# Kernel optimization log

Hardware: AMD Instinct MI355X
Metric: run time of the kernel (lower is better)

Reference implementation:

```python
import jax, jax.numpy as jnp
import numpy as np

ALPHA = 1.0 / 10.0  # dt / tau

def setup_inputs() -> dict:
    key = jax.random.key(0)
    ks = jax.random.split(key, 5)
    seq_len, batch, input_dim, hidden = 256, 128, 256, 1024
    return {
        "input": jax.random.normal(ks[0], (seq_len, batch, input_dim), dtype=jnp.float32),
        "W_in": jax.random.normal(ks[1], (hidden, input_dim), dtype=jnp.float32) / np.sqrt(input_dim),
        "b_in": jax.random.normal(ks[2], (hidden,), dtype=jnp.float32) * 0.01,
        "W_hh": jax.random.normal(ks[3], (hidden, hidden), dtype=jnp.float32) / np.sqrt(hidden),
        "b_hh": jax.random.normal(ks[4], (hidden,), dtype=jnp.float32) * 0.01,
        "h0": jnp.zeros((hidden,), dtype=jnp.float32),
    }

def reference(input, W_in, b_in, W_hh, b_hh, h0):
    # input: [T, B, I] -> states: [T, B, H]
    # Precompute input projections for all timesteps (linear, same math as per-step).
    x_proj = jnp.einsum('tbi,hi->tbh', input, W_in) + b_in  # [T, B, H]
    h_init = jnp.broadcast_to(h0, (input.shape[1], h0.shape[0]))  # [B, H]

    def step(h, xp):
        rec = h @ W_hh.T + b_hh                       # [B, H]
        h_new = (1.0 - ALPHA) * h + ALPHA * (rec + xp)  # leaky integration (noise sigma = 0)
        h_new = jax.nn.relu(h_new)
        return h_new, h_new

    _, states = jax.lax.scan(step, h_init, x_proj)
    return states  # [T, B, H]
```

## Files before the change

### kernel.cpp

```cpp
#include <hip/hip_runtime.h>
#include <hip/hip_bf16.h>

#define T_LEN 256
#define B_DIM 128
#define I_DIM 256
#define H_DIM 1024

typedef __attribute__((ext_vector_type(8))) short short8;
typedef __attribute__((ext_vector_type(4))) float f32x4;

__device__ unsigned g_sync[256];

static __device__ __forceinline__ unsigned short f2bf(float f) {
  unsigned u = __float_as_uint(f);
  return (unsigned short)((u + 0x7fffu + ((u >> 16) & 1u)) >> 16);
}

__global__ __launch_bounds__(256) void xproj_gemm(
    const float* __restrict__ A, const float* __restrict__ W,
    const float* __restrict__ bias, float* __restrict__ C) {
  __shared__ float As[64][33];
  __shared__ float Ws[64][33];

  const int tid = threadIdx.x;
  const int m0 = blockIdx.y * 64;
  const int n0 = blockIdx.x * 64;
  const int ty = tid >> 4;
  const int tx = tid & 15;
  const int r   = tid >> 3;
  const int c4  = (tid & 7) << 2;

  float acc[4][4] = {};

  for (int kc = 0; kc < I_DIM; kc += 32) {
#pragma unroll
    for (int p = 0; p < 2; ++p) {
      const int rr = r + p * 32;
      const float4 a = *(const float4*)(A + (size_t)(m0 + rr) * I_DIM + kc + c4);
      As[rr][c4 + 0] = a.x; As[rr][c4 + 1] = a.y;
      As[rr][c4 + 2] = a.z; As[rr][c4 + 3] = a.w;
      const float4 w = *(const float4*)(W + (size_t)(n0 + rr) * I_DIM + kc + c4);
      Ws[rr][c4 + 0] = w.x; Ws[rr][c4 + 1] = w.y;
      Ws[rr][c4 + 2] = w.z; Ws[rr][c4 + 3] = w.w;
    }
    __syncthreads();
#pragma unroll
    for (int k = 0; k < 32; ++k) {
      float av[4], wv[4];
#pragma unroll
      for (int i = 0; i < 4; ++i) av[i] = As[ty * 4 + i][k];
#pragma unroll
      for (int j = 0; j < 4; ++j) wv[j] = Ws[tx * 4 + j][k];
#pragma unroll
      for (int i = 0; i < 4; ++i)
#pragma unroll
        for (int j = 0; j < 4; ++j)
          acc[i][j] = fmaf(av[i], wv[j], acc[i][j]);
    }
    __syncthreads();
  }

  const float4 bv = *(const float4*)(bias + n0 + tx * 4);
#pragma unroll
  for (int i = 0; i < 4; ++i) {
    float4 o;
    o.x = acc[i][0] + bv.x;
    o.y = acc[i][1] + bv.y;
    o.z = acc[i][2] + bv.z;
    o.w = acc[i][3] + bv.w;
    *(float4*)(C + (size_t)(m0 + ty * 4 + i) * H_DIM + n0 + tx * 4) = o;
  }
}

__global__ __launch_bounds__(256) void cvt_w_bf16(
    const float* __restrict__ W, unsigned short* __restrict__ Wb) {
  const int i4 = blockIdx.x * 256 + threadIdx.x;
  const float4 w = ((const float4*)W)[i4];
  ushort4 o;
  o.x = f2bf(w.x); o.y = f2bf(w.y); o.z = f2bf(w.z); o.w = f2bf(w.w);
  ((ushort4*)Wb)[i4] = o;
}

__global__ __launch_bounds__(256) void init_hT0(
    const float* __restrict__ h0, unsigned short* __restrict__ hT) {
  const int idx = blockIdx.x * 256 + threadIdx.x;
  hT[idx] = f2bf(h0[idx & (H_DIM - 1)]);
  if (blockIdx.x == 0) g_sync[threadIdx.x] = 0u;
}

__global__ __launch_bounds__(256, 1) void rnn_persist(
    unsigned short* __restrict__ hT,
    const unsigned short* __restrict__ Wb,
    const float* __restrict__ b_hh,
    const float* __restrict__ h0,
    float* __restrict__ out)
{
  __shared__ float red[2][16][33];

  const int tid  = threadIdx.x;
  const int wv   = tid >> 6;
  const int lane = tid & 63;
  const int ln   = lane & 15;
  const int q    = lane >> 4;

  const int bid = blockIdx.x;
  const int bq  = bid >> 5;
  const int lj  = bid & 31;
  const int j0  = lj * 32;
  const int mt  = wv & 1;
  const int kh  = wv >> 1;
  const int b0  = bq * 32 + mt * 16;

  short8 wfrag[2][16];
#pragma unroll
  for (int jf = 0; jf < 2; ++jf) {
    const short8* __restrict__ wb8 =
        (const short8*)(Wb + (size_t)(j0 + jf * 16 + ln) * H_DIM + kh * 512 + q * 8);
#pragma unroll
    for (int kc = 0; kc < 16; ++kc) wfrag[jf][kc] = wb8[kc * 4];
  }

  const size_t HT = (size_t)B_DIM * H_DIM;
  const size_t arow = (size_t)(b0 + ln) * H_DIM + kh * 512 + q * 8;
  const unsigned short* __restrict__ ha0 = hT + arow;
  const unsigned short* __restrict__ ha1 = hT + HT + arow;

  float bj[2];
#pragma unroll
  for (int jf = 0; jf < 2; ++jf) bj[jf] = b_hh[j0 + jf * 16 + ln];

  const size_t obase = (size_t)(b0 + q * 4) * H_DIM + j0 + ln;

  float hcur[2][4];
#pragma unroll
  for (int jf = 0; jf < 2; ++jf) {
    const float h0j = h0[j0 + jf * 16 + ln];
#pragma unroll
    for (int r = 0; r < 4; ++r) hcur[jf][r] = h0j;
  }

  unsigned* flags = &g_sync[bq * 32];
  unsigned* epoch = &g_sync[128 + bq * 32];

  for (int t = 0; t < T_LEN; ++t) {
#pragma unroll
    for (int jf = 0; jf < 2; ++jf)
#pragma unroll
      for (int kc = 0; kc < 16; ++kc) asm volatile("" : "+v"(wfrag[jf][kc]));

    float* __restrict__ xio_t = out + (size_t)t * HT;

    float xpv[2][4];
    if (wv < 2) {
#pragma unroll
      for (int jf = 0; jf < 2; ++jf)
#pragma unroll
        for (int r = 0; r < 4; ++r)
          xpv[jf][r] = xio_t[obase + (size_t)r * H_DIM + jf * 16];
    }

    const unsigned short* __restrict__ ha = (t & 1) ? ha1 : ha0;
    short8 hfrag[16];
#pragma unroll
    for (int kc = 0; kc < 16; ++kc) {
      asm volatile("global_load_dwordx4 %0, %1, off offset:%2 sc0 sc1"
                   : "=&v"(hfrag[kc]) : "v"(ha), "i"(kc * 64));
    }
    asm volatile("s_waitcnt vmcnt(0)" ::: "memory");
    __builtin_amdgcn_sched_barrier(0);

    f32x4 a0[2], a1[2];
#pragma unroll
    for (int jf = 0; jf < 2; ++jf) { a0[jf] = (f32x4){0,0,0,0}; a1[jf] = (f32x4){0,0,0,0}; }
#pragma unroll
    for (int kc = 0; kc < 16; kc += 2) {
#pragma unroll
      for (int jf = 0; jf < 2; ++jf) {
        a0[jf] = __builtin_amdgcn_mfma_f32_16x16x32_bf16(hfrag[kc],     wfrag[jf][kc],     a0[jf], 0, 0, 0);
        a1[jf] = __builtin_amdgcn_mfma_f32_16x16x32_bf16(hfrag[kc + 1], wfrag[jf][kc + 1], a1[jf], 0, 0, 0);
      }
    }
    f32x4 acc[2];
#pragma unroll
    for (int jf = 0; jf < 2; ++jf) acc[jf] = a0[jf] + a1[jf];

    if (wv >= 2) {
#pragma unroll
      for (int jf = 0; jf < 2; ++jf)
#pragma unroll
        for (int r = 0; r < 4; ++r) red[mt][q * 4 + r][jf * 16 + ln] = acc[jf][r];
    }
    __syncthreads();
    if (wv < 2) {
      unsigned short* __restrict__ hnext = hT + (size_t)((t + 1) & 1) * HT;
#pragma unroll
      for (int jf = 0; jf < 2; ++jf)
#pragma unroll
        for (int r = 0; r < 4; ++r) {
          const float rec = acc[jf][r] + red[mt][q * 4 + r][jf * 16 + ln];
          float v = 0.9f * hcur[jf][r] + 0.1f * (rec + bj[jf] + xpv[jf][r]);
          v = v > 0.f ? v : 0.f;
          hcur[jf][r] = v;
          const size_t oidx = obase + (size_t)r * H_DIM + jf * 16;
          xio_t[oidx] = v;
          __hip_atomic_store(&hnext[oidx], f2bf(v), __ATOMIC_RELAXED,
                             __HIP_MEMORY_SCOPE_AGENT);
        }
    }
    __syncthreads();

    const unsigned tgt = (unsigned)(t + 1);
    if (lj == 0) {
      if (wv == 0) {
        if (lane == 0)
          __hip_atomic_store(&flags[0], tgt, __ATOMIC_RELAXED,
                             __HIP_MEMORY_SCOPE_AGENT);
        unsigned* fp = &flags[lane & 31];
        for (;;) {
          unsigned fv;
          asm volatile("global_load_dword %0, %1, off sc0 sc1\n\t"
                       "s_waitcnt vmcnt(0)"
                       : "=v"(fv) : "v"(fp) : "memory");
          if (__all((int)fv >= (int)tgt)) break;
          __builtin_amdgcn_s_sleep(1);
        }
        if (lane == 0)
          __hip_atomic_store(epoch, tgt, __ATOMIC_RELAXED,
                             __HIP_MEMORY_SCOPE_AGENT);
      }
    } else if (tid == 0) {
      __hip_atomic_store(&flags[lj], tgt, __ATOMIC_RELAXED,
                         __HIP_MEMORY_SCOPE_AGENT);
      for (;;) {
        unsigned ev;
        asm volatile("global_load_dword %0, %1, off sc0 sc1\n\t"
                     "s_waitcnt vmcnt(0)"
                     : "=v"(ev) : "v"(epoch) : "memory");
        if (ev >= tgt) break;
        __builtin_amdgcn_s_sleep(1);
      }
    }
    __syncthreads();
  }
}

extern "C" void kernel_launch(void* const* d_in, const int* in_sizes, int n_in,
                              void* d_out, int out_size, void* d_ws, size_t ws_size,
                              hipStream_t stream) {
  const float* input = (const float*)d_in[0];
  const float* W_in  = (const float*)d_in[1];
  const float* b_in  = (const float*)d_in[2];
  const float* W_hh  = (const float*)d_in[3];
  const float* b_hh  = (const float*)d_in[4];
  const float* h0    = (const float*)d_in[5];
  float* out = (float*)d_out;

  unsigned short* Wb = (unsigned short*)d_ws;
  unsigned short* hT = Wb + (1 << 20);

  cvt_w_bf16<<<(H_DIM * H_DIM / 4) / 256, 256, 0, stream>>>(W_hh, Wb);
  init_hT0<<<(B_DIM * H_DIM) / 256, 256, 0, stream>>>(h0, hT);

  dim3 g1(H_DIM / 64, (T_LEN * B_DIM) / 64);
  xproj_gemm<<<g1, 256, 0, stream>>>(input, W_in, b_in, out);

  {
    unsigned short* hT_ = hT;
    const unsigned short* Wb_ = Wb;
    const float* bhh_ = b_hh;
    const float* h0_ = h0;
    float* out_ = out;
    void* pargs[5] = {(void*)&hT_, (void*)&Wb_, (void*)&bhh_, (void*)&h0_, (void*)&out_};
    hipLaunchCooperativeKernel((const void*)rnn_persist, dim3(128), dim3(256),
                               pargs, 0, stream);
  }
}
```

Baseline: 1.643 ms.

## Use split-bf16 MFMA for input projection and decentralize step barrier

The input projection GEMM moves from scalar fp32 FMA to MFMA on bf16 hi/lo split operands, using three products to keep near-fp32 accuracy. This path is taken only when the workspace is large enough, and it adds two conversion kernels. The recurrent kernel also drops its two-level barrier (leader gathers flags and publishes an epoch). Instead, each block publishes its own flag and, at the start of the next step, polls all 32 peer flags in its batch group. That removes one barrier stage and the trailing __syncthreads from each timestep.

```diff
diff --git a/kernel.cpp b/kernel.cpp
--- a/kernel.cpp
+++ b/kernel.cpp
@@ -14,6 +14,9 @@
 static __device__ __forceinline__ unsigned short f2bf(float f) {
   unsigned u = __float_as_uint(f);
   return (unsigned short)((u + 0x7fffu + ((u >> 16) & 1u)) >> 16);
+}
+static __device__ __forceinline__ float bf2f(unsigned short h) {
+  return __uint_as_float((unsigned)h << 16);
 }
 
 __global__ __launch_bounds__(256) void xproj_gemm(
@@ -72,6 +75,74 @@
   }
 }
 
+__global__ __launch_bounds__(256) void cvt_hi_lo(
+    const float* __restrict__ X, unsigned short* __restrict__ Xh,
+    unsigned short* __restrict__ Xl) {
+  const int i4 = blockIdx.x * 256 + threadIdx.x;
+  const float4 x = ((const float4*)X)[i4];
+  ushort4 h, l;
+  h.x = f2bf(x.x); l.x = f2bf(x.x - bf2f(h.x));
+  h.y = f2bf(x.y); l.y = f2bf(x.y - bf2f(h.y));
+  h.z = f2bf(x.z); l.z = f2bf(x.z - bf2f(h.z));
+  h.w = f2bf(x.w); l.w = f2bf(x.w - bf2f(h.w));
+  ((ushort4*)Xh)[i4] = h;
+  ((ushort4*)Xl)[i4] = l;
+}
+
+__global__ __launch_bounds__(256) void xproj_mfma(
+    const unsigned short* __restrict__ Ah, const unsigned short* __restrict__ Al,
+    const unsigned short* __restrict__ Wh, const unsigned short* __restrict__ Wl,
+    const float* __restrict__ bias, float* __restrict__ C) {
+  const int tid  = threadIdx.x;
+  const int wv   = tid >> 6;
+  const int lane = tid & 63;
+  const int ln   = lane & 15;
+  const int q    = lane >> 4;
+  const int mw   = wv >> 1;
+  const int nw   = wv & 1;
+  const int m0   = blockIdx.y * 128 + mw * 64;
+  const int n0   = blockIdx.x * 64  + nw * 32;
+
+  f32x4 acc[4][2] = {};
+
+#pragma unroll
+  for (int kc = 0; kc < 8; ++kc) {
+    const int ko = kc * 32 + q * 8;
+    short8 afh[4], afl[4], wfh[2], wfl[2];
+#pragma unroll
+    for (int fm = 0; fm < 4; ++fm) {
+      const size_t off = (size_t)(m0 + fm * 16 + ln) * I_DIM + ko;
+      afh[fm] = *(const short8*)(Ah + off);
+      afl[fm] = *(const short8*)(Al + off);
+    }
+#pragma unroll
+    for (int fn = 0; fn < 2; ++fn) {
+      const size_t off = (size_t)(n0 + fn * 16 + ln) * I_DIM + ko;
+      wfh[fn] = *(const short8*)(Wh + off);
+      wfl[fn] = *(const short8*)(Wl + off);
+    }
+#pragma unroll
+    for (int fm = 0; fm < 4; ++fm)
+#pragma unroll
+      for (int fn = 0; fn < 2; ++fn) {
+        acc[fm][fn] = __builtin_amdgcn_mfma_f32_16x16x32_bf16(afh[fm], wfh[fn], acc[fm][fn], 0, 0, 0);
+        acc[fm][fn] = __builtin_amdgcn_mfma_f32_16x16x32_bf16(afh[fm], wfl[fn], acc[fm][fn], 0, 0, 0);
+        acc[fm][fn] = __builtin_amdgcn_mfma_f32_16x16x32_bf16(afl[fm], wfh[fn], acc[fm][fn], 0, 0, 0);
+      }
+  }
+
+#pragma unroll
+  for (int fn = 0; fn < 2; ++fn) {
+    const int j = n0 + fn * 16 + ln;
+    const float bj = bias[j];
+#pragma unroll
+    for (int fm = 0; fm < 4; ++fm)
+#pragma unroll
+      for (int r = 0; r < 4; ++r)
+        C[(size_t)(m0 + fm * 16 + q * 4 + r) * H_DIM + j] = acc[fm][fn][r] + bj;
+  }
+}
+
 __global__ __launch_bounds__(256) void cvt_w_bf16(
     const float* __restrict__ W, unsigned short* __restrict__ Wb) {
   const int i4 = blockIdx.x * 256 + threadIdx.x;
@@ -140,7 +211,8 @@
   }
 
   unsigned* flags = &g_sync[bq * 32];
-  unsigned* epoch = &g_sync[128 + bq * 32];
+  unsigned* myflag = &g_sync[bq * 32 + lj];
+  unsigned* pollp  = &g_sync[bq * 32 + kh * 16 + ln];
 
   for (int t = 0; t < T_LEN; ++t) {
 #pragma unroll
@@ -158,6 +230,19 @@
         for (int r = 0; r < 4; ++r)
           xpv[jf][r] = xio_t[obase + (size_t)r * H_DIM + jf * 16];
     }
+
+    if (t > 0) {
+      const unsigned tgt = (unsigned)t;
+      for (;;) {
+        unsigned fv;
+        asm volatile("global_load_dword %0, %1, off sc0 sc1\n\t"
+                     "s_waitcnt vmcnt(0)"
+                     : "=v"(fv) : "v"(pollp) : "memory");
+        if (__all((int)fv >= (int)tgt)) break;
+        __builtin_amdgcn_s_sleep(1);
+      }
+    }
+    __builtin_amdgcn_sched_barrier(0);
 
     const unsigned short* __restrict__ ha = (t & 1) ? ha1 : ha0;
     short8 hfrag[16];
@@ -208,40 +293,11 @@
         }
     }
     __syncthreads();
-
-    const unsigned tgt = (unsigned)(t + 1);
-    if (lj == 0) {
-      if (wv == 0) {
-        if (lane == 0)
-          __hip_atomic_store(&flags[0], tgt, __ATOMIC_RELAXED,
-                             __HIP_MEMORY_SCOPE_AGENT);
-        unsigned* fp = &flags[lane & 31];
-        for (;;) {
-          unsigned fv;
-          asm volatile("global_load_dword %0, %1, off sc0 sc1\n\t"
-                       "s_waitcnt vmcnt(0)"
-                       : "=v"(fv) : "v"(fp) : "memory");
-          if (__all((int)fv >= (int)tgt)) break;
-          __builtin_amdgcn_s_sleep(1);
-        }
-        if (lane == 0)
-          __hip_atomic_store(epoch, tgt, __ATOMIC_RELAXED,
-                             __HIP_MEMORY_SCOPE_AGENT);
-      }
-    } else if (tid == 0) {
-      __hip_atomic_store(&flags[lj], tgt, __ATOMIC_RELAXED,
+    if (tid == 0)
+      __hip_atomic_store(myflag, (unsigned)(t + 1), __ATOMIC_RELAXED,
                          __HIP_MEMORY_SCOPE_AGENT);
-      for (;;) {
-        unsigned ev;
-        asm volatile("global_load_dword %0, %1, off sc0 sc1\n\t"
-                     "s_waitcnt vmcnt(0)"
-                     : "=v"(ev) : "v"(epoch) : "memory");
-        if (ev >= tgt) break;
-        __builtin_amdgcn_s_sleep(1);
-      }
-    }
-    __syncthreads();
-  }
+  }
+  (void)flags;
 }
 
 extern "C" void kernel_launch(void* const* d_in, const int* in_sizes, int n_in,
@@ -255,14 +311,26 @@
   const float* h0    = (const float*)d_in[5];
   float* out = (float*)d_out;
 
-  unsigned short* Wb = (unsigned short*)d_ws;
-  unsigned short* hT = Wb + (1 << 20);
+  char* ws = (char*)d_ws;
+  unsigned short* Wb  = (unsigned short*)ws;
+  unsigned short* hT  = (unsigned short*)(ws + (2u << 20));
+  unsigned short* Wih = (unsigned short*)(ws + (5u << 19));
+  unsigned short* Wil = (unsigned short*)(ws + (3u << 20));
+  unsigned short* Ah  = (unsigned short*)(ws + (4u << 20));
+  unsigned short* Al  = (unsigned short*)(ws + (20u << 20));
 
   cvt_w_bf16<<<(H_DIM * H_DIM / 4) / 256, 256, 0, stream>>>(W_hh, Wb);
   init_hT0<<<(B_DIM * H_DIM) / 256, 256, 0, stream>>>(h0, hT);
 
-  dim3 g1(H_DIM / 64, (T_LEN * B_DIM) / 64);
-  xproj_gemm<<<g1, 256, 0, stream>>>(input, W_in, b_in, out);
+  if (ws_size >= (36u << 20)) {
+    cvt_hi_lo<<<(T_LEN * B_DIM * I_DIM / 4) / 256, 256, 0, stream>>>(input, Ah, Al);
+    cvt_hi_lo<<<(H_DIM * I_DIM / 4) / 256, 256, 0, stream>>>(W_in, Wih, Wil);
+    dim3 g1(H_DIM / 64, (T_LEN * B_DIM) / 128);
+    xproj_mfma<<<g1, 256, 0, stream>>>(Ah, Al, Wih, Wil, b_in, out);
+  } else {
+    dim3 g1(H_DIM / 64, (T_LEN * B_DIM) / 64);
+    xproj_gemm<<<g1, 256, 0, stream>>>(input, W_in, b_in, out);
+  }
 
   {
     unsigned short* hT_ = hT;
```

Result: faster. 1.552 ms (-5.5%).
